# Kernel tuning notes

Hardware: AMD Instinct MI355X
Metric: run time of the kernel (lower is better)

The kernel has to match this reference:

```python
import jax, jax.numpy as jnp
import numpy as np

B, N, F, D, H = 4, 2048, 128, 128, 4

def setup_inputs() -> dict:
    key = jax.random.key(0)
    k1, k2, k3, k4 = jax.random.split(key, 4)
    X = jax.random.normal(k1, (B, N, F), dtype=jnp.float32)
    A = jax.random.uniform(k2, (B, N, N), dtype=jnp.float32)
    kernel = jax.random.normal(k3, (F, D), dtype=jnp.float32) * 0.05
    bias = jnp.ones((D,), dtype=jnp.float32)
    attn = jax.random.normal(k4, (H, D, D), dtype=jnp.float32) * 0.05
    return {"X": X, "A": A, "kernel": kernel, "bias": bias, "attn": attn}

def reference(X, A, kernel, bias, attn):
    # Linear projection: [B,N,F] @ [F,D] + bias -> [B,N,D]
    Xp = jnp.einsum('bnf,fd->bnd', X, kernel) + bias
    # Per-head bilinear scores Xp @ attn_h @ Xp^T, batched over heads: [B,H,N,N]
    scores = jnp.einsum('bnd,hde,bme->bhnm', Xp, attn, Xp)
    # Adjacency mask + tanh (fused elementwise)
    Am = jnp.tanh(A[:, None, :, :] * scores)
    # Weighted aggregate per head: [B,H,N,N] @ [B,N,D] -> [B,H,N,D]
    heads = jnp.einsum('bhnm,bmd->bhnd', Am, Xp)
    # Mean over heads, relu
    Xh = jax.nn.relu(jnp.mean(heads, axis=1))
    # Skip connection (shapes match since F == D): relu(Xh + X)
    out = jax.nn.relu(Xh + X)
    return out
```

## Files before the change

kernel.cpp:

```cpp
#include <hip/hip_runtime.h>

#define NB 4
#define NN 2048
#define ND 128
#define NH 4

typedef short short8 __attribute__((ext_vector_type(8)));
typedef short short4v __attribute__((ext_vector_type(4)));
typedef float floatx4 __attribute__((ext_vector_type(4)));

__device__ __forceinline__ short f2bf(float f){
  unsigned u = __float_as_uint(f);
  u += 0x7FFFu + ((u >> 16) & 1u);
  return (short)(u >> 16);
}
__device__ __forceinline__ float bf2f(short s){
  unsigned u = ((unsigned)(unsigned short)s) << 16;
  return __uint_as_float(u);
}

__global__ __launch_bounds__(256) void k1_xp(const float* __restrict__ X,
                                             const float* __restrict__ W,
                                             const float* __restrict__ bias,
                                             short* __restrict__ Xp,
                                             short* __restrict__ XpT){
  int bid = blockIdx.x;
  int b = bid >> 5, i0 = (bid & 31) << 6;
  int t = threadIdx.x, w = t >> 6, lane = t & 63, lq = lane >> 4, lc = lane & 15;
  __shared__ __align__(16) short ldsB[16384];
  #pragma unroll 16
  for (int k = 0; k < 64; ++k){
    int idx = k * 256 + t; int f = idx >> 7, d = idx & 127;
    ldsB[((f >> 3) * 128 + d) * 8 + (f & 7)] = f2bf(W[idx]);
  }
  short8 af[4][4];
  #pragma unroll
  for (int ib = 0; ib < 4; ++ib)
    #pragma unroll
    for (int k = 0; k < 4; ++k){
      const float* xp = &X[(b * NN + i0 + ib * 16 + lc) * ND + k * 32 + lq * 8];
      float4 x0 = *(const float4*)xp;
      float4 x1 = *(const float4*)(xp + 4);
      short8 s;
      s[0]=f2bf(x0.x); s[1]=f2bf(x0.y); s[2]=f2bf(x0.z); s[3]=f2bf(x0.w);
      s[4]=f2bf(x1.x); s[5]=f2bf(x1.y); s[6]=f2bf(x1.z); s[7]=f2bf(x1.w);
      af[ib][k] = s;
    }
  __syncthreads();
  floatx4 acc[4][2];
  #pragma unroll
  for (int ib = 0; ib < 4; ++ib)
    #pragma unroll
    for (int eb = 0; eb < 2; ++eb) acc[ib][eb] = (floatx4){0.f, 0.f, 0.f, 0.f};
  #pragma unroll
  for (int eb = 0; eb < 2; ++eb)
    #pragma unroll
    for (int k = 0; k < 4; ++k){
      short8 bf = *(short8*)&ldsB[(k * 4 + lq) * 1024 + (w * 32 + eb * 16 + lc) * 8];
      #pragma unroll
      for (int ib = 0; ib < 4; ++ib)
        acc[ib][eb] = __builtin_amdgcn_mfma_f32_16x16x32_bf16(af[ib][k], bf, acc[ib][eb], 0, 0, 0);
    }
  __syncthreads();
  short* tr = ldsB;
  #pragma unroll
  for (int ib = 0; ib < 4; ++ib)
    #pragma unroll
    for (int eb = 0; eb < 2; ++eb){
      int d = w * 32 + eb * 16 + lc;
      float bv = bias[d];
      #pragma unroll
      for (int r = 0; r < 4; ++r){
        int n = i0 + ib * 16 + lq * 4 + r;
        short s = f2bf(acc[ib][eb][r] + bv);
        Xp[(b * NN + n) * ND + d] = s;
        tr[d * 72 + (n - i0)] = s;
      }
    }
  __syncthreads();
  #pragma unroll
  for (int c = 0; c < 4; ++c){
    int g = c * 256 + t; int d = g >> 3, n8 = g & 7;
    short8 v;
    #pragma unroll
    for (int j = 0; j < 8; ++j) v[j] = tr[d * 72 + n8 * 8 + j];
    *(short8*)&XpT[(b * ND + d) * NN + i0 + n8 * 8] = v;
  }
}

__global__ __launch_bounds__(256) void k2_y(const short* __restrict__ Xp,
                                            const float* __restrict__ attn,
                                            short* __restrict__ Y){
  int bid = blockIdx.x;
  int it = bid & 31, h = (bid >> 5) & 3, b = bid >> 7;
  int i0 = it << 6;
  int t = threadIdx.x, w = t >> 6, lane = t & 63, lq = lane >> 4, lc = lane & 15;
  __shared__ __align__(16) short ldsB[16384];
  const float* Asrc = attn + h * 16384;
  #pragma unroll 16
  for (int k = 0; k < 64; ++k){
    int idx = k * 256 + t; int dd = idx >> 7, e = idx & 127;
    ldsB[((dd >> 3) * 128 + e) * 8 + (dd & 7)] = f2bf(Asrc[idx]);
  }
  short8 af[4][4];
  #pragma unroll
  for (int ib = 0; ib < 4; ++ib)
    #pragma unroll
    for (int k = 0; k < 4; ++k)
      af[ib][k] = *(const short8*)&Xp[(b * NN + i0 + ib * 16 + lc) * ND + k * 32 + lq * 8];
  __syncthreads();
  floatx4 acc[4][2];
  #pragma unroll
  for (int ib = 0; ib < 4; ++ib)
    #pragma unroll
    for (int eb = 0; eb < 2; ++eb) acc[ib][eb] = (floatx4){0.f, 0.f, 0.f, 0.f};
  #pragma unroll
  for (int eb = 0; eb < 2; ++eb)
    #pragma unroll
    for (int k = 0; k < 4; ++k){
      short8 bf = *(short8*)&ldsB[(k * 4 + lq) * 1024 + (w * 32 + eb * 16 + lc) * 8];
      #pragma unroll
      for (int ib = 0; ib < 4; ++ib)
        acc[ib][eb] = __builtin_amdgcn_mfma_f32_16x16x32_bf16(af[ib][k], bf, acc[ib][eb], 0, 0, 0);
    }
  #pragma unroll
  for (int ib = 0; ib < 4; ++ib)
    #pragma unroll
    for (int eb = 0; eb < 2; ++eb){
      int e = w * 32 + eb * 16 + lc;
      #pragma unroll
      for (int r = 0; r < 4; ++r){
        int n = i0 + ib * 16 + lq * 4 + r;
        Y[((b * NH + h) * NN + n) * ND + e] = f2bf(acc[ib][eb][r]);
      }
    }
}

__global__ __launch_bounds__(256, 4) void k3_fused(const short* __restrict__ Xp,
                                                   const short* __restrict__ XpT,
                                                   const short* __restrict__ Y,
                                                   const float* __restrict__ A,
                                                   float* __restrict__ part){
  int bid = blockIdx.x;
  int it = bid & 127, b = (bid >> 7) & 3, ms = bid >> 9;
  int i0 = it << 4;
  int t = threadIdx.x, w = t >> 6, lane = t & 63, lq = lane >> 4, lc = lane & 15;

  __shared__ __align__(16) short ldsY[8192];
  __shared__ __align__(16) short ldsXpT[8320];
  __shared__ __align__(16) short ldsPh[1024];
  __shared__ __align__(16) short ldsPl[1024];

  #pragma unroll
  for (int c = 0; c < 4; ++c){
    int slot = c * 256 + t;
    int h = slot >> 8, i = (slot >> 4) & 15, d8 = slot & 15;
    short8 v = *(const short8*)&Y[((b * NH + h) * NN + i0 + i) * ND + d8 * 8];
    *(short8*)&ldsY[h * 2048 + i * 128 + ((d8 ^ (i & 7)) << 3)] = v;
  }

  floatx4 acc[2];
  acc[0] = (floatx4){0.f,0.f,0.f,0.f};
  acc[1] = (floatx4){0.f,0.f,0.f,0.f};

  const int mbase = ms << 9;
  const int poff = (w * 2 + (lq >> 1)) * 128 + lc * 8 + (lq & 1) * 4;

  __syncthreads();

  for (int itn = 0; itn < 8; ++itn){
    int m0 = mbase + itn * 64;
    if (itn) __syncthreads();
    const short* src = XpT + b * (ND * NN) + m0;
    #pragma unroll
    for (int c = 0; c < 4; ++c){
      int q = c * 256 + t; int d = q >> 3, mb = q & 7;
      *(short8*)&ldsXpT[mb * 1040 + d * 8] = *(const short8*)&src[d * NN + mb * 8];
    }
    short8 xpf[4];
    const short* xr = Xp + (b * NN + m0 + w * 16 + lc) * ND;
    #pragma unroll
    for (int k = 0; k < 4; ++k) xpf[k] = *(const short8*)&xr[k * 32 + lq * 8];
    floatx4 av = *(const floatx4*)&A[(size_t)(b * NN + i0 + lc) * NN + m0 + w * 16 + lq * 4];

    float psum[4] = {0.f, 0.f, 0.f, 0.f};
    #pragma unroll
    for (int h = 0; h < 4; ++h){
      floatx4 S = (floatx4){0.f,0.f,0.f,0.f};
      #pragma unroll
      for (int k = 0; k < 4; ++k){
        short8 yfr = *(short8*)&ldsY[h * 2048 + lc * 128 + (((k * 4 + lq) ^ (lc & 7)) << 3)];
        S = __builtin_amdgcn_mfma_f32_16x16x32_bf16(xpf[k], yfr, S, 0, 0, 0);
      }
      #pragma unroll
      for (int r = 0; r < 4; ++r){
        float x = av[r] * S[r];
        float e = __builtin_amdgcn_exp2f(x * 2.885390081777926f);
        psum[r] += 1.f - 2.f * __builtin_amdgcn_rcpf(e + 1.f);
      }
    }
    short4v hi4, lo4;
    #pragma unroll
    for (int r = 0; r < 4; ++r){
      float pb = 0.25f * psum[r];
      short h16 = f2bf(pb);
      hi4[r] = h16;
      lo4[r] = f2bf(pb - bf2f(h16));
    }
    *(short4v*)&ldsPh[poff] = hi4;
    *(short4v*)&ldsPl[poff] = lo4;
    __syncthreads();

    #pragma unroll
    for (int kb = 0; kb < 2; ++kb){
      short8 ph = *(short8*)&ldsPh[(kb * 4 + lq) * 128 + lc * 8];
      short8 pl = *(short8*)&ldsPl[(kb * 4 + lq) * 128 + lc * 8];
      #pragma unroll
      for (int db = 0; db < 2; ++db){
        short8 bfr = *(short8*)&ldsXpT[(kb * 4 + lq) * 1040 + (w * 32 + db * 16 + lc) * 8];
        acc[db] = __builtin_amdgcn_mfma_f32_16x16x32_bf16(ph, bfr, acc[db], 0, 0, 0);
        acc[db] = __builtin_amdgcn_mfma_f32_16x16x32_bf16(pl, bfr, acc[db], 0, 0, 0);
      }
    }
  }
  float* dst = part + (size_t)ms * 1048576 + (b * NN + i0) * ND;
  #pragma unroll
  for (int db = 0; db < 2; ++db)
    #pragma unroll
    for (int r = 0; r < 4; ++r)
      dst[(lq * 4 + r) * ND + w * 32 + db * 16 + lc] = acc[db][r];
}

__global__ void k4_final(const float* __restrict__ part, const float* __restrict__ X,
                         float* __restrict__ out){
  int f = (blockIdx.x * 256 + threadIdx.x) * 4;
  float4 s0 = *(const float4*)(part + f);
  float4 s1 = *(const float4*)(part + 1048576 + f);
  float4 s2 = *(const float4*)(part + 2097152 + f);
  float4 s3 = *(const float4*)(part + 3145728 + f);
  float4 xv = *(const float4*)(X + f);
  float4 o;
  o.x = fmaxf(fmaxf(s0.x + s1.x + s2.x + s3.x, 0.f) + xv.x, 0.f);
  o.y = fmaxf(fmaxf(s0.y + s1.y + s2.y + s3.y, 0.f) + xv.y, 0.f);
  o.z = fmaxf(fmaxf(s0.z + s1.z + s2.z + s3.z, 0.f) + xv.z, 0.f);
  o.w = fmaxf(fmaxf(s0.w + s1.w + s2.w + s3.w, 0.f) + xv.w, 0.f);
  *(float4*)(out + f) = o;
}

extern "C" void kernel_launch(void* const* d_in, const int* in_sizes, int n_in,
                              void* d_out, int out_size, void* d_ws, size_t ws_size,
                              hipStream_t stream) {
  const float* X    = (const float*)d_in[0];
  const float* A    = (const float*)d_in[1];
  const float* W    = (const float*)d_in[2];
  const float* bias = (const float*)d_in[3];
  const float* attn = (const float*)d_in[4];
  float* out = (float*)d_out;

  const size_t OFF_XP    = 0;
  const size_t OFF_XPT   = (size_t)2 << 20;
  const size_t OFF_Y     = (size_t)4 << 20;
  const size_t OFF_PART  = (size_t)12 << 20;
  const size_t NEED = (size_t)28 << 20;
  if (ws_size < NEED) return;

  char* ws = (char*)d_ws;
  short* Xp    = (short*)(ws + OFF_XP);
  short* XpT   = (short*)(ws + OFF_XPT);
  short* Y     = (short*)(ws + OFF_Y);
  float* part  = (float*)(ws + OFF_PART);

  k1_xp<<<128, 256, 0, stream>>>(X, W, bias, Xp, XpT);
  k2_y<<<512, 256, 0, stream>>>(Xp, attn, Y);
  k3_fused<<<2048, 256, 0, stream>>>(Xp, XpT, Y, A, part);
  k4_final<<<1024, 256, 0, stream>>>(part, X, out);
}
```

Measured before the change: 166.4 us.

## Process two 16-row i-tiles per block in fused kernel to reuse Xp/XpT loads

Each k3 block now handles 32 output rows (two 16-row tiles) instead of 16, so the XpT tile staged in LDS and the Xp fragments loaded per m-chunk are reused across both tiles. The grid is halved and the LDS Y buffer and P buffers are doubled. Launch bounds drop to 2 blocks per SM. This trades fewer global and LDS loads per unit of work for higher register and LDS use, lower occupancy, and less latency hiding.

```diff
diff --git a/kernel.cpp b/kernel.cpp
--- a/kernel.cpp
+++ b/kernel.cpp
@@ -136,32 +136,34 @@
     }
 }
 
-__global__ __launch_bounds__(256, 4) void k3_fused(const short* __restrict__ Xp,
+__global__ __launch_bounds__(256, 2) void k3_fused(const short* __restrict__ Xp,
                                                    const short* __restrict__ XpT,
                                                    const short* __restrict__ Y,
                                                    const float* __restrict__ A,
                                                    float* __restrict__ part){
   int bid = blockIdx.x;
-  int it = bid & 127, b = (bid >> 7) & 3, ms = bid >> 9;
-  int i0 = it << 4;
+  int it = bid & 63, b = (bid >> 6) & 3, ms = bid >> 8;
+  int i0 = it << 5;
   int t = threadIdx.x, w = t >> 6, lane = t & 63, lq = lane >> 4, lc = lane & 15;
 
-  __shared__ __align__(16) short ldsY[8192];
+  __shared__ __align__(16) short ldsY[16384];
   __shared__ __align__(16) short ldsXpT[8320];
-  __shared__ __align__(16) short ldsPh[1024];
-  __shared__ __align__(16) short ldsPl[1024];
-
-  #pragma unroll
-  for (int c = 0; c < 4; ++c){
+  __shared__ __align__(16) short ldsPh[2][1024];
+  __shared__ __align__(16) short ldsPl[2][1024];
+
+  #pragma unroll
+  for (int c = 0; c < 8; ++c){
     int slot = c * 256 + t;
-    int h = slot >> 8, i = (slot >> 4) & 15, d8 = slot & 15;
-    short8 v = *(const short8*)&Y[((b * NH + h) * NN + i0 + i) * ND + d8 * 8];
-    *(short8*)&ldsY[h * 2048 + i * 128 + ((d8 ^ (i & 7)) << 3)] = v;
-  }
-
-  floatx4 acc[2];
-  acc[0] = (floatx4){0.f,0.f,0.f,0.f};
-  acc[1] = (floatx4){0.f,0.f,0.f,0.f};
+    int tl = slot >> 10, h = (slot >> 8) & 3, i = (slot >> 4) & 15, d8 = slot & 15;
+    short8 v = *(const short8*)&Y[((b * NH + h) * NN + i0 + tl * 16 + i) * ND + d8 * 8];
+    *(short8*)&ldsY[tl * 8192 + h * 2048 + i * 128 + ((d8 ^ (i & 7)) << 3)] = v;
+  }
+
+  floatx4 acc[2][2];
+  #pragma unroll
+  for (int tl = 0; tl < 2; ++tl)
+    #pragma unroll
+    for (int db = 0; db < 2; ++db) acc[tl][db] = (floatx4){0.f,0.f,0.f,0.f};
 
   const int mbase = ms << 9;
   const int poff = (w * 2 + (lq >> 1)) * 128 + lc * 8 + (lq & 1) * 4;
@@ -181,54 +183,69 @@
     const short* xr = Xp + (b * NN + m0 + w * 16 + lc) * ND;
     #pragma unroll
     for (int k = 0; k < 4; ++k) xpf[k] = *(const short8*)&xr[k * 32 + lq * 8];
-    floatx4 av = *(const floatx4*)&A[(size_t)(b * NN + i0 + lc) * NN + m0 + w * 16 + lq * 4];
-
-    float psum[4] = {0.f, 0.f, 0.f, 0.f};
-    #pragma unroll
-    for (int h = 0; h < 4; ++h){
-      floatx4 S = (floatx4){0.f,0.f,0.f,0.f};
-      #pragma unroll
-      for (int k = 0; k < 4; ++k){
-        short8 yfr = *(short8*)&ldsY[h * 2048 + lc * 128 + (((k * 4 + lq) ^ (lc & 7)) << 3)];
-        S = __builtin_amdgcn_mfma_f32_16x16x32_bf16(xpf[k], yfr, S, 0, 0, 0);
-      }
+    floatx4 av[2];
+    #pragma unroll
+    for (int tl = 0; tl < 2; ++tl)
+      av[tl] = *(const floatx4*)&A[(size_t)(b * NN + i0 + tl * 16 + lc) * NN
+                                   + m0 + w * 16 + lq * 4];
+
+    #pragma unroll
+    for (int tl = 0; tl < 2; ++tl){
+      float psum[4] = {0.f, 0.f, 0.f, 0.f};
+      #pragma unroll
+      for (int h = 0; h < 4; ++h){
+        floatx4 S = (floatx4){0.f,0.f,0.f,0.f};
+        #pragma unroll
+        for (int k = 0; k < 4; ++k){
+          short8 yfr = *(short8*)&ldsY[tl * 8192 + h * 2048 + lc * 128
+                                       + (((k * 4 + lq) ^ (lc & 7)) << 3)];
+          S = __builtin_amdgcn_mfma_f32_16x16x32_bf16(xpf[k], yfr, S, 0, 0, 0);
+        }
+        #pragma unroll
+        for (int r = 0; r < 4; ++r){
+          float x = av[tl][r] * S[r];
+          float e = __builtin_amdgcn_exp2f(x * 2.885390081777926f);
+          psum[r] += 1.f - 2.f * __builtin_amdgcn_rcpf(e + 1.f);
+        }
+      }
+      short4v hi4, lo4;
       #pragma unroll
       for (int r = 0; r < 4; ++r){
-        float x = av[r] * S[r];
-        float e = __builtin_amdgcn_exp2f(x * 2.885390081777926f);
-        psum[r] += 1.f - 2.f * __builtin_amdgcn_rcpf(e + 1.f);
-      }
-    }
-    short4v hi4, lo4;
-    #pragma unroll
-    for (int r = 0; r < 4; ++r){
-      float pb = 0.25f * psum[r];
-      short h16 = f2bf(pb);
-      hi4[r] = h16;
-      lo4[r] = f2bf(pb - bf2f(h16));
-    }
-    *(short4v*)&ldsPh[poff] = hi4;
-    *(short4v*)&ldsPl[poff] = lo4;
+        float pb = 0.25f * psum[r];
+        short h16 = f2bf(pb);
+        hi4[r] = h16;
+        lo4[r] = f2bf(pb - bf2f(h16));
+      }
+      *(short4v*)&ldsPh[tl][poff] = hi4;
+      *(short4v*)&ldsPl[tl][poff] = lo4;
+    }
     __syncthreads();
 
     #pragma unroll
     for (int kb = 0; kb < 2; ++kb){
-      short8 ph = *(short8*)&ldsPh[(kb * 4 + lq) * 128 + lc * 8];
-      short8 pl = *(short8*)&ldsPl[(kb * 4 + lq) * 128 + lc * 8];
+      short8 ph0 = *(short8*)&ldsPh[0][(kb * 4 + lq) * 128 + lc * 8];
+      short8 pl0 = *(short8*)&ldsPl[0][(kb * 4 + lq) * 128 + lc * 8];
+      short8 ph1 = *(short8*)&ldsPh[1][(kb * 4 + lq) * 128 + lc * 8];
+      short8 pl1 = *(short8*)&ldsPl[1][(kb * 4 + lq) * 128 + lc * 8];
       #pragma unroll
       for (int db = 0; db < 2; ++db){
         short8 bfr = *(short8*)&ldsXpT[(kb * 4 + lq) * 1040 + (w * 32 + db * 16 + lc) * 8];
-        acc[db] = __builtin_amdgcn_mfma_f32_16x16x32_bf16(ph, bfr, acc[db], 0, 0, 0);
-        acc[db] = __builtin_amdgcn_mfma_f32_16x16x32_bf16(pl, bfr, acc[db], 0, 0, 0);
-      }
-    }
-  }
-  float* dst = part + (size_t)ms * 1048576 + (b * NN + i0) * ND;
-  #pragma unroll
-  for (int db = 0; db < 2; ++db)
-    #pragma unroll
-    for (int r = 0; r < 4; ++r)
-      dst[(lq * 4 + r) * ND + w * 32 + db * 16 + lc] = acc[db][r];
+        acc[0][db] = __builtin_amdgcn_mfma_f32_16x16x32_bf16(ph0, bfr, acc[0][db], 0, 0, 0);
+        acc[0][db] = __builtin_amdgcn_mfma_f32_16x16x32_bf16(pl0, bfr, acc[0][db], 0, 0, 0);
+        acc[1][db] = __builtin_amdgcn_mfma_f32_16x16x32_bf16(ph1, bfr, acc[1][db], 0, 0, 0);
+        acc[1][db] = __builtin_amdgcn_mfma_f32_16x16x32_bf16(pl1, bfr, acc[1][db], 0, 0, 0);
+      }
+    }
+  }
+  #pragma unroll
+  for (int tl = 0; tl < 2; ++tl){
+    float* dst = part + (size_t)ms * 1048576 + (size_t)(b * NN + i0 + tl * 16) * ND;
+    #pragma unroll
+    for (int db = 0; db < 2; ++db)
+      #pragma unroll
+      for (int r = 0; r < 4; ++r)
+        dst[(lq * 4 + r) * ND + w * 32 + db * 16 + lc] = acc[tl][db][r];
+  }
 }
 
 __global__ void k4_final(const float* __restrict__ part, const float* __restrict__ X,
@@ -272,6 +289,6 @@
 
   k1_xp<<<128, 256, 0, stream>>>(X, W, bias, Xp, XpT);
   k2_y<<<512, 256, 0, stream>>>(Xp, attn, Y);
-  k3_fused<<<2048, 256, 0, stream>>>(Xp, XpT, Y, A, part);
+  k3_fused<<<1024, 256, 0, stream>>>(Xp, XpT, Y, A, part);
   k4_final<<<1024, 256, 0, stream>>>(part, X, out);
 }
```

New measurement: 163.5 us. About the same (-1.8%).
